# Kernel tuning notes

Measured on AMD Instinct MI355X. Metric: run time of the kernel, lower is better.

The kernel has to match this reference:

```python
import jax, jax.numpy as jnp
import numpy as np

S, N, MSA_DIM, PAIR_DIM, D, H = 8, 256, 256, 128, 32, 8
EPS = 1e-5


def layer_norm(x, w, b):
    mu = jnp.mean(x, axis=-1, keepdims=True)
    var = jnp.mean((x - mu) ** 2, axis=-1, keepdims=True)
    return (x - mu) * jax.lax.rsqrt(var + EPS) * w + b


def setup_inputs() -> dict:
    key = jax.random.key(0)
    ks = jax.random.split(key, 8)
    def rnd(k, shape, scale=1.0):
        return jax.random.normal(k, shape, jnp.float32) * scale
    return {
        "msa_rep": rnd(ks[0], (S, N, MSA_DIM)),
        "pair_rep": rnd(ks[1], (N, N, PAIR_DIM)),
        "ln_w": jnp.ones((MSA_DIM,), jnp.float32),
        "ln_b": jnp.zeros((MSA_DIM,), jnp.float32),
        "w_qkv": rnd(ks[2], (MSA_DIM, 3 * H * D), 0.02),
        "ln_pair_w": jnp.ones((PAIR_DIM,), jnp.float32),
        "ln_pair_b": jnp.zeros((PAIR_DIM,), jnp.float32),
        "w_b": rnd(ks[3], (PAIR_DIM, H), 0.02),
        "w_g": rnd(ks[4], (MSA_DIM, H * D), 0.02),
        "w_out": rnd(ks[5], (H * D, MSA_DIM), 0.02),
        "b_out": jnp.zeros((MSA_DIM,), jnp.float32),
    }


def reference(msa_rep, pair_rep, ln_w, ln_b, w_qkv, ln_pair_w, ln_pair_b,
              w_b, w_g, w_out, b_out):
    s, n, _ = msa_rep.shape
    x = layer_norm(msa_rep, ln_w, ln_b)                      # [s, n, msa_dim]
    qkv = x @ w_qkv                                          # [s, n, 3*h*d]
    # chunk(3, dim=-1) then view(..., d, h): d outer, h inner
    q, k, v = [t.reshape(s, n, D, H) for t in jnp.split(qkv, 3, axis=-1)]
    # pair bias: LN + linear -> [n, n, h], broadcast to [1, i, j, 1, h]
    b = layer_norm(pair_rep, ln_pair_w, ln_pair_b) @ w_b     # [n, n, h]
    g = jax.nn.sigmoid(x @ w_g).reshape(s, n, D, H)          # gate [s, n, d, h]
    # NOTE: logits keep the d axis (no contraction): einsum 'sidh,sjdh->sijdh'
    scores = (q[:, :, None, :, :] * k[:, None, :, :, :]) * (D ** -0.5) \
             + b[None, :, :, None, :]                        # [s, i, j, d, h]
    a = jax.nn.softmax(scores, axis=2)                       # softmax over j
    out = g * jnp.einsum('sijdh,sjdh->sidh', a, v)           # [s, n, d, h]
    return out.reshape(s, n, D * H) @ w_out + b_out          # [s, n, msa_dim]
```

## Files before the change

### kernel.cpp

```cpp
#include <hip/hip_runtime.h>
#include <math.h>

#define S_DIM 8
#define N_RES 256
#define MSA_DIM 256
#define PAIR_DIM 128
#define D_DIM 32
#define H_DIM 8
#define M_ROWS (S_DIM * N_RES)
#define QKV_N (3 * H_DIM * D_DIM)
#define HD (H_DIM * D_DIM)
#define XW_N 1024
#define LOG2E 1.4426950408889634f

typedef __attribute__((ext_vector_type(8))) short short8;
typedef __attribute__((ext_vector_type(4))) float floatx4;

#define DPP_ADD(x, ctrl, rmask)                                                \
    x += __int_as_float(__builtin_amdgcn_update_dpp(                           \
        0, __float_as_int(x), (ctrl), (rmask), 0xf, true))

__device__ __forceinline__ float wave_sum63(float x) {
    DPP_ADD(x, 0x111, 0xf);
    DPP_ADD(x, 0x112, 0xf);
    DPP_ADD(x, 0x114, 0xf);
    DPP_ADD(x, 0x118, 0xf);
    DPP_ADD(x, 0x142, 0xa);
    DPP_ADD(x, 0x143, 0xc);
    return x;
}

__device__ __forceinline__ float quad_sum(float x) {
    x += __int_as_float(__builtin_amdgcn_update_dpp(
        0, __float_as_int(x), 0xB1, 0xf, 0xf, true));
    x += __int_as_float(__builtin_amdgcn_update_dpp(
        0, __float_as_int(x), 0x4E, 0xf, 0xf, true));
    return x;
}

__device__ __forceinline__ unsigned short bf16rn(float v) {
    unsigned u = __float_as_uint(v);
    return (unsigned short)((u + 0x7FFF + ((u >> 16) & 1)) >> 16);
}

__global__ __launch_bounds__(256) void prep_kernel(
    const float* __restrict__ w_qkv, const float* __restrict__ w_g,
    unsigned short* __restrict__ whiT, unsigned short* __restrict__ wloT,
    const float* __restrict__ w_out,
    unsigned short* __restrict__ wouthiT, unsigned short* __restrict__ woutloT,
    const float* __restrict__ msa, const float* __restrict__ lnw,
    const float* __restrict__ lnb, unsigned short* __restrict__ xhi,
    unsigned short* __restrict__ xlo)
{
    int b = blockIdx.x;
    int t = threadIdx.x;

    {
        int wv = t >> 6, l = t & 63;
        int row = b * 4 + wv;
        float4 v4 = *(const float4*)&msa[(size_t)row * 256 + l * 4];
        float s1 = v4.x + v4.y + v4.z + v4.w;
        float s2 = v4.x * v4.x + v4.y * v4.y + v4.z * v4.z + v4.w * v4.w;
        s1 = wave_sum63(s1);
        s2 = wave_sum63(s2);
        float S1 = __int_as_float(__builtin_amdgcn_readlane(__float_as_int(s1), 63));
        float S2 = __int_as_float(__builtin_amdgcn_readlane(__float_as_int(s2), 63));
        float mu = S1 * (1.0f / 256.0f);
        float var = S2 * (1.0f / 256.0f) - mu * mu;
        float rs = rsqrtf(var + 1e-5f);
        float4 w4 = *(const float4*)&lnw[l * 4];
        float4 bb4 = *(const float4*)&lnb[l * 4];
        float y[4];
        y[0] = (v4.x - mu) * rs * w4.x + bb4.x;
        y[1] = (v4.y - mu) * rs * w4.y + bb4.y;
        y[2] = (v4.z - mu) * rs * w4.z + bb4.z;
        y[3] = (v4.w - mu) * rs * w4.w + bb4.w;
        unsigned short hh[4], ll[4];
#pragma unroll
        for (int i = 0; i < 4; i++) {
            hh[i] = bf16rn(y[i]);
            ll[i] = bf16rn(y[i] - __uint_as_float((unsigned)hh[i] << 16));
        }
        uint2 ph, pl;
        ph.x = (unsigned)hh[0] | ((unsigned)hh[1] << 16);
        ph.y = (unsigned)hh[2] | ((unsigned)hh[3] << 16);
        pl.x = (unsigned)ll[0] | ((unsigned)ll[1] << 16);
        pl.y = (unsigned)ll[2] | ((unsigned)ll[3] << 16);
        *(uint2*)&xhi[(size_t)row * 256 + l * 4] = ph;
        *(uint2*)&xlo[(size_t)row * 256 + l * 4] = pl;
    }

    if (t < 64) {
        int id = b * 64 + t;
        int n = id >> 5, oct = id & 31, k0 = oct * 8;
        const float* src;
        int stride;
        if (n < QKV_N) { src = w_qkv + n; stride = QKV_N; }
        else           { src = w_g + (n - QKV_N); stride = HD; }
        unsigned short h8[8], l8[8];
#pragma unroll
        for (int j = 0; j < 8; j++) {
            float v = src[(size_t)(k0 + j) * stride];
            unsigned short h = bf16rn(v);
            h8[j] = h;
            l8[j] = bf16rn(v - __uint_as_float((unsigned)h << 16));
        }
        *(short8*)&whiT[n * 256 + k0] = *(short8*)h8;
        *(short8*)&wloT[n * 256 + k0] = *(short8*)l8;
    } else if (t < 80) {
        int id = b * 16 + (t - 64);
        int n = id >> 5, oct = id & 31, k0 = oct * 8;
        unsigned short h8[8], l8[8];
#pragma unroll
        for (int j = 0; j < 8; j++) {
            int k = k0 + j;
            int wrow = (k & 31) * 8 + (k >> 5);
            float v = w_out[(size_t)wrow * 256 + n];
            unsigned short h = bf16rn(v);
            h8[j] = h;
            l8[j] = bf16rn(v - __uint_as_float((unsigned)h << 16));
        }
        *(short8*)&wouthiT[n * 256 + k0] = *(short8*)h8;
        *(short8*)&woutloT[n * 256 + k0] = *(short8*)l8;
    }
}

__global__ __launch_bounds__(256) void mid_kernel(
    const float* __restrict__ pair, const float* __restrict__ lw,
    const float* __restrict__ lb, const float* __restrict__ wb,
    float* __restrict__ b2,
    const unsigned short* __restrict__ xhi, const unsigned short* __restrict__ xlo,
    const unsigned short* __restrict__ whiT, const unsigned short* __restrict__ wloT,
    float* __restrict__ q_t, float* __restrict__ k_t,
    float* __restrict__ v_t, float* __restrict__ g_t)
{
    __shared__ __align__(16) char smem[54272];
    int bx = blockIdx.x;
    int t = threadIdx.x;
    int g3 = bx / 3, r3 = bx - g3 * 3;

    if (r3 != 2) {
        float* As = (float*)smem;
        float* Spart = (float*)smem + 1552;
        float* Qpart = (float*)smem + 1816;
        int pair_id = g3 * 2 + r3;
        if (t < 128) {
            float lwc = lw[t];
#pragma unroll
            for (int h = 0; h < 8; h++)
                As[t * 12 + h] = lwc * wb[t * 8 + h] * LOG2E;
        }
        __syncthreads();
        {
            int h = t >> 5, seg = t & 31, cbase = seg * 4;
            float sa = 0, sq = 0;
#pragma unroll
            for (int cc = 0; cc < 4; cc++) {
                int c = cbase + cc;
                sa += As[c * 12 + h];
                sq += lb[c] * wb[c * 8 + h];
            }
            Spart[h * 33 + seg] = sa;
            Qpart[h * 33 + seg] = sq * LOG2E;
        }
        __syncthreads();
        if (t < 8) {
            float s = 0, q = 0;
#pragma unroll
            for (int j = 0; j < 32; j++) {
                s += Spart[t * 33 + j];
                q += Qpart[t * 33 + j];
            }
            As[1536 + t] = s;
            As[1544 + t] = q;
        }
        __syncthreads();
        int row = pair_id * 64 + (t >> 2);
        int q = t & 3;
        const float* in = pair + (size_t)row * PAIR_DIM;
        float4 x4[8];
#pragma unroll
        for (int it = 0; it < 8; it++)
            x4[it] = *(const float4*)&in[it * 16 + q * 4];
        float s = 0, s2 = 0;
        float dot[8] = {};
#pragma unroll
        for (int it = 0; it < 8; it++) {
            float xk[4];
            *(float4*)xk = x4[it];
#pragma unroll
            for (int k = 0; k < 4; k++) {
                int c = it * 16 + q * 4 + k;
                float xv = xk[k];
                s += xv; s2 += xv * xv;
                float4 A0 = *(const float4*)&As[c * 12];
                float4 A1 = *(const float4*)&As[c * 12 + 4];
                dot[0] += xv * A0.x; dot[1] += xv * A0.y;
                dot[2] += xv * A0.z; dot[3] += xv * A0.w;
                dot[4] += xv * A1.x; dot[5] += xv * A1.y;
                dot[6] += xv * A1.z; dot[7] += xv * A1.w;
            }
        }
        s = quad_sum(s);
        s2 = quad_sum(s2);
#pragma unroll
        for (int h = 0; h < 8; h++) dot[h] = quad_sum(dot[h]);
        float mu = s * (1.0f / 128.0f);
        float var = s2 * (1.0f / 128.0f) - mu * mu;
        float rs = rsqrtf(var + 1e-5f);
        int h0 = q * 2;
#pragma unroll
        for (int u = 0; u < 2; u++) {
            int h = h0 + u;
            b2[h * 65536 + row] = rs * (dot[h] - mu * As[1536 + h]) + As[1544 + h];
        }
    } else {
        unsigned short* Ahi = (unsigned short*)smem;
        unsigned short* Alo = Ahi + 64 * 72;
        unsigned short* Bhi = Alo + 64 * 72;
        unsigned short* Blo = Bhi + 64 * 72;
        float* Cs = (float*)(smem + 4 * 9216);
        int gid = g3;
        int n0 = (gid & 15) * 64, m0 = (gid >> 4) * 64;
        int w = t >> 6, L = t & 63;
        int wm = (w & 1) * 32, wn = (w >> 1) * 32;
        int l15 = L & 15, l4 = L >> 4;
        int am = t >> 3, ak = (t & 7) * 8;
        int bn0 = t >> 3, bn1 = (t + 256) >> 3;
        int bc = (t & 7) * 8;
        floatx4 acc[2][2];
#pragma unroll
        for (int a = 0; a < 2; a++)
#pragma unroll
            for (int c = 0; c < 2; c++) acc[a][c] = (floatx4){0, 0, 0, 0};

        short8 rahi0 = *(const short8*)&xhi[(m0 + am) * 256 + ak];
        short8 rahi1 = *(const short8*)&xhi[(m0 + am + 32) * 256 + ak];
        short8 ralo0 = *(const short8*)&xlo[(m0 + am) * 256 + ak];
        short8 ralo1 = *(const short8*)&xlo[(m0 + am + 32) * 256 + ak];
        short8 rbhi0 = *(const short8*)&whiT[(n0 + bn0) * 256 + bc];
        short8 rbhi1 = *(const short8*)&whiT[(n0 + bn1) * 256 + bc];
        short8 rblo0 = *(const short8*)&wloT[(n0 + bn0) * 256 + bc];
        short8 rblo1 = *(const short8*)&wloT[(n0 + bn1) * 256 + bc];

        for (int kb = 0; kb < 4; kb++) {
            __syncthreads();
            *(short8*)&Ahi[am * 72 + ak] = rahi0;
            *(short8*)&Ahi[(am + 32) * 72 + ak] = rahi1;
            *(short8*)&Alo[am * 72 + ak] = ralo0;
            *(short8*)&Alo[(am + 32) * 72 + ak] = ralo1;
            *(short8*)&Bhi[bn0 * 72 + bc] = rbhi0;
            *(short8*)&Bhi[bn1 * 72 + bc] = rbhi1;
            *(short8*)&Blo[bn0 * 72 + bc] = rblo0;
            *(short8*)&Blo[bn1 * 72 + bc] = rblo1;
            __syncthreads();
            if (kb < 3) {
                int kB = (kb + 1) * 64;
                rahi0 = *(const short8*)&xhi[(m0 + am) * 256 + kB + ak];
                rahi1 = *(const short8*)&xhi[(m0 + am + 32) * 256 + kB + ak];
                ralo0 = *(const short8*)&xlo[(m0 + am) * 256 + kB + ak];
                ralo1 = *(const short8*)&xlo[(m0 + am + 32) * 256 + kB + ak];
                rbhi0 = *(const short8*)&whiT[(n0 + bn0) * 256 + kB + bc];
                rbhi1 = *(const short8*)&whiT[(n0 + bn1) * 256 + kB + bc];
                rblo0 = *(const short8*)&wloT[(n0 + bn0) * 256 + kB + bc];
                rblo1 = *(const short8*)&wloT[(n0 + bn1) * 256 + kB + bc];
            }
#pragma unroll
            for (int pass = 0; pass < 3; pass++) {
                const unsigned short* Ab = (pass == 1) ? Alo : Ahi;
                const unsigned short* Bb = (pass == 2) ? Blo : Bhi;
#pragma unroll
                for (int ks = 0; ks < 2; ks++) {
                    int ko = ks * 32 + l4 * 8;
                    short8 af[2], bf[2];
#pragma unroll
                    for (int a = 0; a < 2; a++)
                        af[a] = *(short8*)&Ab[(wm + a * 16 + l15) * 72 + ko];
#pragma unroll
                    for (int c = 0; c < 2; c++)
                        bf[c] = *(short8*)&Bb[(wn + c * 16 + l15) * 72 + ko];
#pragma unroll
                    for (int a = 0; a < 2; a++)
#pragma unroll
                        for (int c = 0; c < 2; c++)
                            acc[a][c] = __builtin_amdgcn_mfma_f32_16x16x32_bf16(
                                af[a], bf[c], acc[a][c], 0, 0, 0);
                }
            }
        }
#pragma unroll
        for (int a = 0; a < 2; a++)
#pragma unroll
            for (int c = 0; c < 2; c++) {
                int nl = wn + c * 16 + l15;
#pragma unroll
                for (int rg = 0; rg < 4; rg++) {
                    int ml = wm + a * 16 + l4 * 4 + rg;
                    Cs[ml * 68 + nl] = acc[a][c][rg];
                }
            }
        __syncthreads();
        int qkv_mode = (n0 < QKV_N);
        int chunk = n0 >> 8;
        int dbase = (n0 & 255) >> 3;
#pragma unroll
        for (int j = 0; j < 4; j++) {
            int id = t + 256 * j;
            int m = id >> 4;
            int h = (id >> 1) & 7;
            int dq = id & 1;
            float vals[4];
#pragma unroll
            for (int jj = 0; jj < 4; jj++)
                vals[jj] = Cs[m * 68 + (dq * 4 + jj) * 8 + h];
            int mm = m0 + m;
            int daddr = dbase + dq * 4;
            if (qkv_mode) {
                float* dst = (chunk == 0) ? q_t : ((chunk == 1) ? k_t : v_t);
                *(float4*)&dst[(size_t)(h * M_ROWS + mm) * D_DIM + daddr] =
                    *(float4*)vals;
            } else {
                float4 o;
                o.x = 1.0f / (1.0f + __expf(-vals[0]));
                o.y = 1.0f / (1.0f + __expf(-vals[1]));
                o.z = 1.0f / (1.0f + __expf(-vals[2]));
                o.w = 1.0f / (1.0f + __expf(-vals[3]));
                *(float4*)&g_t[(size_t)(h * M_ROWS + mm) * D_DIM + daddr] = o;
            }
        }
    }
}

__global__ __launch_bounds__(256) void attn_kernel(
    const float* __restrict__ q_t, const float* __restrict__ k_t,
    const float* __restrict__ v_t, const float* __restrict__ g_t,
    const float* __restrict__ b2, unsigned short* __restrict__ ao_hi,
    unsigned short* __restrict__ ao_lo)
{
    __shared__ float k_sh[256][32];
    __shared__ float v_sh[256][32];
    int blk = blockIdx.x;
    int h = blk & 7, s = (blk >> 3) & 7, it = blk >> 6;
    int t = threadIdx.x;
    const float* kb = k_t + (size_t)(h * M_ROWS + s * N_RES) * D_DIM;
    const float* vb = v_t + (size_t)(h * M_ROWS + s * N_RES) * D_DIM;
    for (int idx = t; idx < 2048; idx += 256) {
        ((float4*)k_sh)[idx] = ((const float4*)kb)[idx];
        ((float4*)v_sh)[idx] = ((const float4*)vb)[idx];
    }
    __syncthreads();
    int jp = t & 3, dg = (t >> 2) & 7, li = t >> 5;
    int d0 = dg * 4;
    const float SCL2 = 0.17677669529663687f * LOG2E;
    int ig[4], mrow[4];
    float qs[4][4];
#pragma unroll
    for (int r = 0; r < 4; r++) {
        ig[r] = it * 32 + r * 8 + li;
        mrow[r] = s * N_RES + ig[r];
        float4 q4 = *(const float4*)&q_t[(size_t)(h * M_ROWS + mrow[r]) * D_DIM + d0];
        qs[r][0] = q4.x * SCL2; qs[r][1] = q4.y * SCL2;
        qs[r][2] = q4.z * SCL2; qs[r][3] = q4.w * SCL2;
    }
    float den[4][4] = {}, acc[4][4] = {};
    const float* bbase = b2 + h * 65536;
    float4 bbv[4];
#pragma unroll
    for (int r = 0; r < 4; r++)
        bbv[r] = *(const float4*)&bbase[ig[r] * 256 + jp * 64];
    for (int js4 = 0; js4 < 16; js4++) {
        float bb[4][4];
#pragma unroll
        for (int r = 0; r < 4; r++)
            *(float4*)&bb[r][0] = bbv[r];
        if (js4 < 15) {
#pragma unroll
            for (int r = 0; r < 4; r++)
                bbv[r] = *(const float4*)&bbase[ig[r] * 256 + jp * 64 + (js4 + 1) * 4];
        }
#pragma unroll
        for (int u = 0; u < 4; u++) {
            int j = jp * 64 + js4 * 4 + u;
            float ka[4], va[4];
            *(float4*)ka = *(const float4*)&k_sh[j][d0];
            *(float4*)va = *(const float4*)&v_sh[j][d0];
#pragma unroll
            for (int r = 0; r < 4; r++) {
#pragma unroll
                for (int c = 0; c < 4; c++) {
                    float e = __builtin_amdgcn_exp2f(qs[r][c] * ka[c] + bb[r][u]);
                    den[r][c] += e;
                    acc[r][c] += e * va[c];
                }
            }
        }
    }
    float4 g4[4];
#pragma unroll
    for (int r = 0; r < 4; r++)
        g4[r] = *(const float4*)&g_t[(size_t)(h * M_ROWS + mrow[r]) * D_DIM + d0];
#pragma unroll
    for (int r = 0; r < 4; r++)
#pragma unroll
        for (int c = 0; c < 4; c++) {
            den[r][c] = quad_sum(den[r][c]);
            acc[r][c] = quad_sum(acc[r][c]);
        }
    if (jp == 0) {
#pragma unroll
        for (int r = 0; r < 4; r++) {
            float o[4];
            o[0] = g4[r].x * acc[r][0] * __builtin_amdgcn_rcpf(den[r][0]);
            o[1] = g4[r].y * acc[r][1] * __builtin_amdgcn_rcpf(den[r][1]);
            o[2] = g4[r].z * acc[r][2] * __builtin_amdgcn_rcpf(den[r][2]);
            o[3] = g4[r].w * acc[r][3] * __builtin_amdgcn_rcpf(den[r][3]);
            unsigned short hi[4], lo[4];
#pragma unroll
            for (int c = 0; c < 4; c++) {
                hi[c] = bf16rn(o[c]);
                lo[c] = bf16rn(o[c] - __uint_as_float((unsigned)hi[c] << 16));
            }
            size_t base = (size_t)mrow[r] * 256 + h * 32 + d0;
            uint2 ph, pl;
            ph.x = (unsigned)hi[0] | ((unsigned)hi[1] << 16);
            ph.y = (unsigned)hi[2] | ((unsigned)hi[3] << 16);
            pl.x = (unsigned)lo[0] | ((unsigned)lo[1] << 16);
            pl.y = (unsigned)lo[2] | ((unsigned)lo[3] << 16);
            *(uint2*)&ao_hi[base] = ph;
            *(uint2*)&ao_lo[base] = pl;
        }
    }
}

__global__ __launch_bounds__(256) void out_mfma_kernel(
    const unsigned short* __restrict__ ahi, const unsigned short* __restrict__ alo,
    const unsigned short* __restrict__ whi, const unsigned short* __restrict__ wlo,
    const float* __restrict__ bias, float* __restrict__ out)
{
    __shared__ unsigned short As[2][16 * 72];
    __shared__ unsigned short Bs[2][64 * 72];
    __shared__ float Cs[16 * 68];
    int t = threadIdx.x;
    int n0 = blockIdx.x * 64, m0 = blockIdx.y * 16;
    int w = t >> 6, L = t & 63;
    int wn = w * 16;
    int l15 = L & 15, l4 = L >> 4;
    int alm = t >> 3, alk = (t & 7) * 8;
    bool doA = (t < 128);
    floatx4 acc = (floatx4){0, 0, 0, 0};

    short8 pa, pb[2];
    if (doA) pa = *(const short8*)&ahi[(m0 + alm) * 256 + alk];
#pragma unroll
    for (int j = 0; j < 2; j++) {
        int id = t + 256 * j;
        int bn = id >> 3, bc = (id & 7) * 8;
        pb[j] = *(const short8*)&whi[(n0 + bn) * 256 + bc];
    }
    if (doA) *(short8*)&As[0][alm * 72 + alk] = pa;
#pragma unroll
    for (int j = 0; j < 2; j++) {
        int id = t + 256 * j;
        int bn = id >> 3, bc = (id & 7) * 8;
        *(short8*)&Bs[0][bn * 72 + bc] = pb[j];
    }

    for (int r = 0; r < 12; r++) {
        if (r < 11) {
            int rn = r + 1;
            int seg = rn >> 2, kb = (rn & 3) * 64;
            const unsigned short* An = (seg == 1) ? alo : ahi;
            const unsigned short* Bn = (seg == 2) ? wlo : whi;
            if (doA) pa = *(const short8*)&An[(m0 + alm) * 256 + kb + alk];
#pragma unroll
            for (int j = 0; j < 2; j++) {
                int id = t + 256 * j;
                int bn = id >> 3, bc = (id & 7) * 8;
                pb[j] = *(const short8*)&Bn[(n0 + bn) * 256 + kb + bc];
            }
        }
        __syncthreads();
        int cur = r & 1;
#pragma unroll
        for (int ks = 0; ks < 2; ks++) {
            int ko = ks * 32 + l4 * 8;
            short8 af = *(short8*)&As[cur][l15 * 72 + ko];
            short8 bf = *(short8*)&Bs[cur][(wn + l15) * 72 + ko];
            acc = __builtin_amdgcn_mfma_f32_16x16x32_bf16(af, bf, acc, 0, 0, 0);
        }
        if (r < 11) {
            int nxt = cur ^ 1;
            if (doA) *(short8*)&As[nxt][alm * 72 + alk] = pa;
#pragma unroll
            for (int j = 0; j < 2; j++) {
                int id = t + 256 * j;
                int bn = id >> 3, bc = (id & 7) * 8;
                *(short8*)&Bs[nxt][bn * 72 + bc] = pb[j];
            }
        }
    }
#pragma unroll
    for (int rg = 0; rg < 4; rg++)
        Cs[(l4 * 4 + rg) * 68 + wn + l15] = acc[rg];
    __syncthreads();
    {
        int m = t >> 4, nc = (t & 15) * 4;
        float4 v = *(float4*)&Cs[m * 68 + nc];
        float4 bb = *(const float4*)&bias[n0 + nc];
        float4 o;
        o.x = v.x + bb.x; o.y = v.y + bb.y;
        o.z = v.z + bb.z; o.w = v.w + bb.w;
        *(float4*)&out[(size_t)(m0 + m) * 256 + n0 + nc] = o;
    }
}

extern "C" void kernel_launch(void* const* d_in, const int* in_sizes, int n_in,
                              void* d_out, int out_size, void* d_ws, size_t ws_size,
                              hipStream_t stream)
{
    const float* msa_rep   = (const float*)d_in[0];
    const float* pair_rep  = (const float*)d_in[1];
    const float* ln_w      = (const float*)d_in[2];
    const float* ln_b      = (const float*)d_in[3];
    const float* w_qkv     = (const float*)d_in[4];
    const float* ln_pair_w = (const float*)d_in[5];
    const float* ln_pair_b = (const float*)d_in[6];
    const float* w_b       = (const float*)d_in[7];
    const float* w_g       = (const float*)d_in[8];
    const float* w_out     = (const float*)d_in[9];
    const float* b_out     = (const float*)d_in[10];
    float* out = (float*)d_out;

    float* ws = (float*)d_ws;
    const size_t CH = 524288;
    float* q_t = ws + 0 * CH;
    float* k_t = ws + 1 * CH;
    float* v_t = ws + 2 * CH;
    float* g_t = ws + 3 * CH;
    float* b2  = ws + 4 * CH;
    unsigned short* ao_hi   = (unsigned short*)(ws + 5 * CH);
    unsigned short* ao_lo   = ao_hi + (size_t)M_ROWS * 256;
    unsigned short* xhi     = (unsigned short*)(ws + 6 * CH);
    unsigned short* xlo     = xhi + (size_t)M_ROWS * 256;
    unsigned short* whiT    = (unsigned short*)(ws + 7 * CH);
    unsigned short* wloT    = whiT + (size_t)XW_N * 256;
    unsigned short* wouthiT = (unsigned short*)(ws + 8 * CH);
    unsigned short* woutloT = wouthiT + 65536;

    prep_kernel<<<512, 256, 0, stream>>>(
        w_qkv, w_g, whiT, wloT,
        w_out, wouthiT, woutloT,
        msa_rep, ln_w, ln_b, xhi, xlo);

    mid_kernel<<<1536, 256, 0, stream>>>(
        pair_rep, ln_pair_w, ln_pair_b, w_b, b2,
        xhi, xlo, whiT, wloT, q_t, k_t, v_t, g_t);

    attn_kernel<<<512, 256, 0, stream>>>(q_t, k_t, v_t, g_t, b2, ao_hi, ao_lo);

    out_mfma_kernel<<<dim3(4, 128), 256, 0, stream>>>(
        ao_hi, ao_lo, wouthiT, woutloT, b_out, out);
}
```

Baseline: 142.6 us.

## Fuse MSA layernorm and weight bf16 split into QKV/gate GEMM kernel

Removes the separate prep kernel. The QKV/gate GEMM blocks now compute layernorm statistics for their 64 rows, then load raw fp32 msa and weights, normalize and split into bf16 hi/lo in registers, overlapping the conversion with the MFMA passes. The w_out conversion moves to 32 extra blocks of mid_kernel. This saves one launch and the round trip of the xhi/xlo and whiT/wloT buffers through memory. In exchange, each GEMM block redoes the layernorm and weight conversion, and it reads weights with strided, uncoalesced column loads.

```diff
diff --git a/kernel.cpp b/kernel.cpp
--- a/kernel.cpp
+++ b/kernel.cpp
@@ -20,16 +20,6 @@
     x += __int_as_float(__builtin_amdgcn_update_dpp(                           \
         0, __float_as_int(x), (ctrl), (rmask), 0xf, true))
 
-__device__ __forceinline__ float wave_sum63(float x) {
-    DPP_ADD(x, 0x111, 0xf);
-    DPP_ADD(x, 0x112, 0xf);
-    DPP_ADD(x, 0x114, 0xf);
-    DPP_ADD(x, 0x118, 0xf);
-    DPP_ADD(x, 0x142, 0xa);
-    DPP_ADD(x, 0x143, 0xc);
-    return x;
-}
-
 __device__ __forceinline__ float quad_sum(float x) {
     x += __int_as_float(__builtin_amdgcn_update_dpp(
         0, __float_as_int(x), 0xB1, 0xf, 0xf, true));
@@ -43,72 +33,36 @@
     return (unsigned short)((u + 0x7FFF + ((u >> 16) & 1)) >> 16);
 }
 
-__global__ __launch_bounds__(256) void prep_kernel(
+__device__ __forceinline__ void cvt_hl8(const float* y, short8& hi, short8& lo) {
+    unsigned short h8[8], l8[8];
+#pragma unroll
+    for (int j = 0; j < 8; j++) {
+        unsigned short h = bf16rn(y[j]);
+        h8[j] = h;
+        l8[j] = bf16rn(y[j] - __uint_as_float((unsigned)h << 16));
+    }
+    hi = *(short8*)h8;
+    lo = *(short8*)l8;
+}
+
+__global__ __launch_bounds__(256) void mid_kernel(
+    const float* __restrict__ pair, const float* __restrict__ lw,
+    const float* __restrict__ lb, const float* __restrict__ wb,
+    float* __restrict__ b2,
+    const float* __restrict__ msa, const float* __restrict__ lnw,
+    const float* __restrict__ lnb,
     const float* __restrict__ w_qkv, const float* __restrict__ w_g,
-    unsigned short* __restrict__ whiT, unsigned short* __restrict__ wloT,
     const float* __restrict__ w_out,
     unsigned short* __restrict__ wouthiT, unsigned short* __restrict__ woutloT,
-    const float* __restrict__ msa, const float* __restrict__ lnw,
-    const float* __restrict__ lnb, unsigned short* __restrict__ xhi,
-    unsigned short* __restrict__ xlo)
+    float* __restrict__ q_t, float* __restrict__ k_t,
+    float* __restrict__ v_t, float* __restrict__ g_t)
 {
-    int b = blockIdx.x;
+    __shared__ __align__(16) char smem[54784];
+    int bx = blockIdx.x;
     int t = threadIdx.x;
 
-    {
-        int wv = t >> 6, l = t & 63;
-        int row = b * 4 + wv;
-        float4 v4 = *(const float4*)&msa[(size_t)row * 256 + l * 4];
-        float s1 = v4.x + v4.y + v4.z + v4.w;
-        float s2 = v4.x * v4.x + v4.y * v4.y + v4.z * v4.z + v4.w * v4.w;
-        s1 = wave_sum63(s1);
-        s2 = wave_sum63(s2);
-        float S1 = __int_as_float(__builtin_amdgcn_readlane(__float_as_int(s1), 63));
-        float S2 = __int_as_float(__builtin_amdgcn_readlane(__float_as_int(s2), 63));
-        float mu = S1 * (1.0f / 256.0f);
-        float var = S2 * (1.0f / 256.0f) - mu * mu;
-        float rs = rsqrtf(var + 1e-5f);
-        float4 w4 = *(const float4*)&lnw[l * 4];
-        float4 bb4 = *(const float4*)&lnb[l * 4];
-        float y[4];
-        y[0] = (v4.x - mu) * rs * w4.x + bb4.x;
-        y[1] = (v4.y - mu) * rs * w4.y + bb4.y;
-        y[2] = (v4.z - mu) * rs * w4.z + bb4.z;
-        y[3] = (v4.w - mu) * rs * w4.w + bb4.w;
-        unsigned short hh[4], ll[4];
-#pragma unroll
-        for (int i = 0; i < 4; i++) {
-            hh[i] = bf16rn(y[i]);
-            ll[i] = bf16rn(y[i] - __uint_as_float((unsigned)hh[i] << 16));
-        }
-        uint2 ph, pl;
-        ph.x = (unsigned)hh[0] | ((unsigned)hh[1] << 16);
-        ph.y = (unsigned)hh[2] | ((unsigned)hh[3] << 16);
-        pl.x = (unsigned)ll[0] | ((unsigned)ll[1] << 16);
-        pl.y = (unsigned)ll[2] | ((unsigned)ll[3] << 16);
-        *(uint2*)&xhi[(size_t)row * 256 + l * 4] = ph;
-        *(uint2*)&xlo[(size_t)row * 256 + l * 4] = pl;
-    }
-
-    if (t < 64) {
-        int id = b * 64 + t;
-        int n = id >> 5, oct = id & 31, k0 = oct * 8;
-        const float* src;
-        int stride;
-        if (n < QKV_N) { src = w_qkv + n; stride = QKV_N; }
-        else           { src = w_g + (n - QKV_N); stride = HD; }
-        unsigned short h8[8], l8[8];
-#pragma unroll
-        for (int j = 0; j < 8; j++) {
-            float v = src[(size_t)(k0 + j) * stride];
-            unsigned short h = bf16rn(v);
-            h8[j] = h;
-            l8[j] = bf16rn(v - __uint_as_float((unsigned)h << 16));
-        }
-        *(short8*)&whiT[n * 256 + k0] = *(short8*)h8;
-        *(short8*)&wloT[n * 256 + k0] = *(short8*)l8;
-    } else if (t < 80) {
-        int id = b * 16 + (t - 64);
+    if (bx >= 1536) {
+        int id = (bx - 1536) * 256 + t;
         int n = id >> 5, oct = id & 31, k0 = oct * 8;
         unsigned short h8[8], l8[8];
 #pragma unroll
@@ -122,21 +76,9 @@
         }
         *(short8*)&wouthiT[n * 256 + k0] = *(short8*)h8;
         *(short8*)&woutloT[n * 256 + k0] = *(short8*)l8;
-    }
-}
-
-__global__ __launch_bounds__(256) void mid_kernel(
-    const float* __restrict__ pair, const float* __restrict__ lw,
-    const float* __restrict__ lb, const float* __restrict__ wb,
-    float* __restrict__ b2,
-    const unsigned short* __restrict__ xhi, const unsigned short* __restrict__ xlo,
-    const unsigned short* __restrict__ whiT, const unsigned short* __restrict__ wloT,
-    float* __restrict__ q_t, float* __restrict__ k_t,
-    float* __restrict__ v_t, float* __restrict__ g_t)
-{
-    __shared__ __align__(16) char smem[54272];
-    int bx = blockIdx.x;
-    int t = threadIdx.x;
+        return;
+    }
+
     int g3 = bx / 3, r3 = bx - g3 * 3;
 
     if (r3 != 2) {
@@ -219,51 +161,113 @@
         unsigned short* Alo = Ahi + 64 * 72;
         unsigned short* Bhi = Alo + 64 * 72;
         unsigned short* Blo = Bhi + 64 * 72;
-        float* Cs = (float*)(smem + 4 * 9216);
+        float* Cs = (float*)(smem + 36864);
+        float* rst = (float*)(smem + 36864 + 17408);
         int gid = g3;
         int n0 = (gid & 15) * 64, m0 = (gid >> 4) * 64;
         int w = t >> 6, L = t & 63;
         int wm = (w & 1) * 32, wn = (w >> 1) * 32;
         int l15 = L & 15, l4 = L >> 4;
         int am = t >> 3, ak = (t & 7) * 8;
-        int bn0 = t >> 3, bn1 = (t + 256) >> 3;
-        int bc = (t & 7) * 8;
+        int bn0 = t >> 3, bn1 = bn0 + 32, bc = (t & 7) * 8;
+
+        {
+            int rrow = t >> 2, q4i = t & 3;
+            const float* mr = msa + (size_t)(m0 + rrow) * 256 + q4i * 64;
+            float s1 = 0, s2 = 0;
+#pragma unroll
+            for (int i = 0; i < 16; i++) {
+                float4 v4 = *(const float4*)&mr[i * 4];
+                s1 += v4.x + v4.y + v4.z + v4.w;
+                s2 += v4.x * v4.x + v4.y * v4.y + v4.z * v4.z + v4.w * v4.w;
+            }
+            s1 = quad_sum(s1);
+            s2 = quad_sum(s2);
+            if (q4i == 0) {
+                float mu = s1 * (1.0f / 256.0f);
+                float var = s2 * (1.0f / 256.0f) - mu * mu;
+                rst[rrow * 2] = mu;
+                rst[rrow * 2 + 1] = rsqrtf(var + 1e-5f);
+            }
+        }
+        __syncthreads();
+        float mu0 = rst[am * 2], rs0 = rst[am * 2 + 1];
+        float mu1 = rst[(am + 32) * 2], rs1 = rst[(am + 32) * 2 + 1];
+
+        const float* bsrc0;
+        const float* bsrc1;
+        int bstr;
+        if (n0 < QKV_N) {
+            bstr = QKV_N;
+            bsrc0 = w_qkv + n0 + bn0;
+            bsrc1 = w_qkv + n0 + bn1;
+        } else {
+            bstr = HD;
+            bsrc0 = w_g + (n0 - QKV_N) + bn0;
+            bsrc1 = w_g + (n0 - QKV_N) + bn1;
+        }
+
         floatx4 acc[2][2];
 #pragma unroll
         for (int a = 0; a < 2; a++)
 #pragma unroll
             for (int c = 0; c < 2; c++) acc[a][c] = (floatx4){0, 0, 0, 0};
 
-        short8 rahi0 = *(const short8*)&xhi[(m0 + am) * 256 + ak];
-        short8 rahi1 = *(const short8*)&xhi[(m0 + am + 32) * 256 + ak];
-        short8 ralo0 = *(const short8*)&xlo[(m0 + am) * 256 + ak];
-        short8 ralo1 = *(const short8*)&xlo[(m0 + am + 32) * 256 + ak];
-        short8 rbhi0 = *(const short8*)&whiT[(n0 + bn0) * 256 + bc];
-        short8 rbhi1 = *(const short8*)&whiT[(n0 + bn1) * 256 + bc];
-        short8 rblo0 = *(const short8*)&wloT[(n0 + bn0) * 256 + bc];
-        short8 rblo1 = *(const short8*)&wloT[(n0 + bn1) * 256 + bc];
+        short8 sa_h0, sa_h1, sa_l0, sa_l1, sb_h0, sb_h1, sb_l0, sb_l1;
+        {
+            float ar0[8], ar1[8], br0[8], br1[8], lwv[8], lbv[8];
+            *(float4*)&ar0[0] = *(const float4*)&msa[(size_t)(m0 + am) * 256 + ak];
+            *(float4*)&ar0[4] = *(const float4*)&msa[(size_t)(m0 + am) * 256 + ak + 4];
+            *(float4*)&ar1[0] = *(const float4*)&msa[(size_t)(m0 + am + 32) * 256 + ak];
+            *(float4*)&ar1[4] = *(const float4*)&msa[(size_t)(m0 + am + 32) * 256 + ak + 4];
+#pragma unroll
+            for (int j = 0; j < 8; j++) {
+                br0[j] = bsrc0[(size_t)(bc + j) * bstr];
+                br1[j] = bsrc1[(size_t)(bc + j) * bstr];
+            }
+            *(float4*)&lwv[0] = *(const float4*)&lnw[ak];
+            *(float4*)&lwv[4] = *(const float4*)&lnw[ak + 4];
+            *(float4*)&lbv[0] = *(const float4*)&lnb[ak];
+            *(float4*)&lbv[4] = *(const float4*)&lnb[ak + 4];
+            float y0[8], y1[8];
+#pragma unroll
+            for (int j = 0; j < 8; j++) {
+                y0[j] = (ar0[j] - mu0) * rs0 * lwv[j] + lbv[j];
+                y1[j] = (ar1[j] - mu1) * rs1 * lwv[j] + lbv[j];
+            }
+            cvt_hl8(y0, sa_h0, sa_l0);
+            cvt_hl8(y1, sa_h1, sa_l1);
+            cvt_hl8(br0, sb_h0, sb_l0);
+            cvt_hl8(br1, sb_h1, sb_l1);
+        }
 
         for (int kb = 0; kb < 4; kb++) {
             __syncthreads();
-            *(short8*)&Ahi[am * 72 + ak] = rahi0;
-            *(short8*)&Ahi[(am + 32) * 72 + ak] = rahi1;
-            *(short8*)&Alo[am * 72 + ak] = ralo0;
-            *(short8*)&Alo[(am + 32) * 72 + ak] = ralo1;
-            *(short8*)&Bhi[bn0 * 72 + bc] = rbhi0;
-            *(short8*)&Bhi[bn1 * 72 + bc] = rbhi1;
-            *(short8*)&Blo[bn0 * 72 + bc] = rblo0;
-            *(short8*)&Blo[bn1 * 72 + bc] = rblo1;
+            *(short8*)&Ahi[am * 72 + ak] = sa_h0;
+            *(short8*)&Ahi[(am + 32) * 72 + ak] = sa_h1;
+            *(short8*)&Alo[am * 72 + ak] = sa_l0;
+            *(short8*)&Alo[(am + 32) * 72 + ak] = sa_l1;
+            *(short8*)&Bhi[bn0 * 72 + bc] = sb_h0;
+            *(short8*)&Bhi[bn1 * 72 + bc] = sb_h1;
+            *(short8*)&Blo[bn0 * 72 + bc] = sb_l0;
+            *(short8*)&Blo[bn1 * 72 + bc] = sb_l1;
             __syncthreads();
+            float ar0[8], ar1[8], br0[8], br1[8], lwv[8], lbv[8];
             if (kb < 3) {
                 int kB = (kb + 1) * 64;
-                rahi0 = *(const short8*)&xhi[(m0 + am) * 256 + kB + ak];
-                rahi1 = *(const short8*)&xhi[(m0 + am + 32) * 256 + kB + ak];
-                ralo0 = *(const short8*)&xlo[(m0 + am) * 256 + kB + ak];
-                ralo1 = *(const short8*)&xlo[(m0 + am + 32) * 256 + kB + ak];
-                rbhi0 = *(const short8*)&whiT[(n0 + bn0) * 256 + kB + bc];
-                rbhi1 = *(const short8*)&whiT[(n0 + bn1) * 256 + kB + bc];
-                rblo0 = *(const short8*)&wloT[(n0 + bn0) * 256 + kB + bc];
-                rblo1 = *(const short8*)&wloT[(n0 + bn1) * 256 + kB + bc];
+                *(float4*)&ar0[0] = *(const float4*)&msa[(size_t)(m0 + am) * 256 + kB + ak];
+                *(float4*)&ar0[4] = *(const float4*)&msa[(size_t)(m0 + am) * 256 + kB + ak + 4];
+                *(float4*)&ar1[0] = *(const float4*)&msa[(size_t)(m0 + am + 32) * 256 + kB + ak];
+                *(float4*)&ar1[4] = *(const float4*)&msa[(size_t)(m0 + am + 32) * 256 + kB + ak + 4];
+#pragma unroll
+                for (int j = 0; j < 8; j++) {
+                    br0[j] = bsrc0[(size_t)(kB + bc + j) * bstr];
+                    br1[j] = bsrc1[(size_t)(kB + bc + j) * bstr];
+                }
+                *(float4*)&lwv[0] = *(const float4*)&lnw[kB + ak];
+                *(float4*)&lwv[4] = *(const float4*)&lnw[kB + ak + 4];
+                *(float4*)&lbv[0] = *(const float4*)&lnb[kB + ak];
+                *(float4*)&lbv[4] = *(const float4*)&lnb[kB + ak + 4];
             }
 #pragma unroll
             for (int pass = 0; pass < 3; pass++) {
@@ -286,6 +290,18 @@
                             acc[a][c] = __builtin_amdgcn_mfma_f32_16x16x32_bf16(
                                 af[a], bf[c], acc[a][c], 0, 0, 0);
                 }
+            }
+            if (kb < 3) {
+                float y0[8], y1[8];
+#pragma unroll
+                for (int j = 0; j < 8; j++) {
+                    y0[j] = (ar0[j] - mu0) * rs0 * lwv[j] + lbv[j];
+                    y1[j] = (ar1[j] - mu1) * rs1 * lwv[j] + lbv[j];
+                }
+                cvt_hl8(y0, sa_h0, sa_l0);
+                cvt_hl8(y1, sa_h1, sa_l1);
+                cvt_hl8(br0, sb_h0, sb_l0);
+                cvt_hl8(br1, sb_h1, sb_l1);
             }
         }
 #pragma unroll
@@ -540,21 +556,15 @@
     float* b2  = ws + 4 * CH;
     unsigned short* ao_hi   = (unsigned short*)(ws + 5 * CH);
     unsigned short* ao_lo   = ao_hi + (size_t)M_ROWS * 256;
-    unsigned short* xhi     = (unsigned short*)(ws + 6 * CH);
-    unsigned short* xlo     = xhi + (size_t)M_ROWS * 256;
-    unsigned short* whiT    = (unsigned short*)(ws + 7 * CH);
-    unsigned short* wloT    = whiT + (size_t)XW_N * 256;
-    unsigned short* wouthiT = (unsigned short*)(ws + 8 * CH);
+    unsigned short* wouthiT = (unsigned short*)(ws + 6 * CH);
     unsigned short* woutloT = wouthiT + 65536;
 
-    prep_kernel<<<512, 256, 0, stream>>>(
-        w_qkv, w_g, whiT, wloT,
+    mid_kernel<<<1568, 256, 0, stream>>>(
+        pair_rep, ln_pair_w, ln_pair_b, w_b, b2,
+        msa_rep, ln_w, ln_b,
+        w_qkv, w_g,
         w_out, wouthiT, woutloT,
-        msa_rep, ln_w, ln_b, xhi, xlo);
-
-    mid_kernel<<<1536, 256, 0, stream>>>(
-        pair_rep, ln_pair_w, ln_pair_b, w_b, b2,
-        xhi, xlo, whiT, wloT, q_t, k_t, v_t, g_t);
+        q_t, k_t, v_t, g_t);
 
     attn_kernel<<<512, 256, 0, stream>>>(q_t, k_t, v_t, g_t, b2, ao_hi, ao_lo);
 
```

Measured after the change: 154.8 us. +8.6%, slower.
